# Optimization experiments

Measured on AMD Instinct MI355X. Metric: run time of the kernel, lower is better.

The kernel has to match this reference:

```python
import jax, jax.numpy as jnp
import numpy as np

B, IN, OUT, RANK = 256, 1024, 1024, 16


def setup_inputs() -> dict:
    key = jax.random.key(0)
    k1, k2, k3, k4 = jax.random.split(key, 4)
    std = (0.02 * RANK ** (-0.5)) ** 0.5
    return {
        "input": jax.random.normal(k1, (B, IN), dtype=jnp.float32),
        "coef": jax.random.normal(k2, (B, RANK), dtype=jnp.float32),
        "weight": jax.random.normal(k3, (OUT, IN, RANK), dtype=jnp.float32) * std,
        "bias": jax.random.normal(k4, (OUT, RANK), dtype=jnp.float32) * 0.02,
    }


def reference(input, coef, weight, bias):
    # Per-sample path of MixtureLinear (coef has shape (B, rank), B > 1):
    # out[b,o] = sum_i input[b,i] * sum_r weight[o,i,r] * coef[b,r]
    #          + sum_r bias[o,r] * coef[b,r]
    # Fused form: contract input with weight first -> (B, out, rank), a tiny
    # intermediate, instead of materializing the (B, out, in) combined weight.
    proj = jnp.einsum('bi,oir->bor', input, weight)   # (B, OUT, RANK)
    out = jnp.einsum('bor,br->bo', proj, coef)         # (B, OUT)
    out = out + jnp.einsum('or,br->bo', bias, coef)
    return out
```

## Files before the change

### kernel.cpp

```cpp
#include <hip/hip_runtime.h>
#include <hip/hip_bf16.h>

#define M 256
#define NOUT 1024
#define KTOT 16384
#define RANK 16
#define NKC 32
#define KCHUNK 512
#define BK 32
#define NPH 16
#define BO 64

typedef __attribute__((ext_vector_type(8)))  short bf16x8_t;
typedef __attribute__((ext_vector_type(4)))  float f32x4_t;
typedef __attribute__((ext_vector_type(16))) float f32x16_t;
typedef __attribute__((ext_vector_type(8)))  unsigned short u16x8_t;

static __device__ __forceinline__ unsigned short f2bf(float f) {
  unsigned u = __builtin_bit_cast(unsigned, f);
  u += 0x7FFFu + ((u >> 16) & 1u);
  return (unsigned short)(u >> 16);
}
static __device__ __forceinline__ float bf2f(unsigned short h) {
  unsigned u = ((unsigned)h) << 16;
  return __builtin_bit_cast(float, u);
}
static __device__ __forceinline__ bf16x8_t cvt8(f32x4_t a, f32x4_t b) {
  bf16x8_t r;
  r[0] = (short)f2bf(a[0]); r[1] = (short)f2bf(a[1]);
  r[2] = (short)f2bf(a[2]); r[3] = (short)f2bf(a[3]);
  r[4] = (short)f2bf(b[0]); r[5] = (short)f2bf(b[1]);
  r[6] = (short)f2bf(b[2]); r[7] = (short)f2bf(b[3]);
  return r;
}

__global__ __launch_bounds__(256) void build_x_kernel(
    const float* __restrict__ input, const float* __restrict__ coef,
    unsigned short* __restrict__ X)
{
  int idx = blockIdx.x * 256 + threadIdx.x;
  int b = idx >> 10, i = idx & 1023;
  float in = input[idx];
  const float* c = coef + b * RANK;
  u16x8_t lo, hi;
  #pragma unroll
  for (int r = 0; r < 8; ++r) lo[r] = f2bf(in * c[r]);
  #pragma unroll
  for (int r = 0; r < 8; ++r) hi[r] = f2bf(in * c[8 + r]);
  int chunk = i >> 1;
  int s0 = (i & 1) * 2;
  int sw = b & 3;
  size_t base = ((size_t)chunk * 256 + b) * 32;
  *(u16x8_t*)(X + base + (size_t)((s0    ) ^ sw) * 8) = lo;
  *(u16x8_t*)(X + base + (size_t)((s0 | 1) ^ sw) * 8) = hi;
}

__global__ __launch_bounds__(512, 2) void gemm_kernel(
    const unsigned short* __restrict__ X, const float* __restrict__ W,
    unsigned short* __restrict__ part)
{
  __shared__ unsigned short Xs0[256 * 4 * 8];
  __shared__ unsigned short Xs1[256 * 4 * 8];
  __shared__ float          Wf0[64 * 8 * 4];
  __shared__ float          Wf1[64 * 8 * 4];

  const int tid = threadIdx.x;
  const int w = tid >> 6, lane = tid & 63;
  const int l31 = lane & 31, l5 = lane >> 5;
  const int ow = w & 1, btp = w >> 1;

  const int lin = blockIdx.x;
  const int idx = lin >> 3;
  const int kc = (lin & 7) * 4 + (idx & 3);
  const int ot = idx >> 2;

  const int o0 = ot * BO;
  const int kb0 = kc * KCHUNK;

  f32x16_t acc0 = (f32x16_t)(0.0f), acc1 = (f32x16_t)(0.0f);

  const int wo_ = tid >> 3, ws_ = tid & 7;
  const float* wsrc = W + (size_t)(o0 + wo_) * KTOT + kb0 + ((ws_ ^ (wo_ & 7)) * 4);
  const unsigned short* xbase = X + (size_t)(kc * NPH) * (256 * 32);

  #define SB __builtin_amdgcn_sched_barrier(0);

  #define STAGE(P, XB, WB)                                                   \
    {                                                                        \
      __builtin_amdgcn_global_load_lds(                                      \
          (const __attribute__((address_space(1))) unsigned int*)            \
              (wsrc + (P) * 32),                                             \
          (__attribute__((address_space(3))) unsigned int*)(&WB[tid * 4]),   \
          16, 0, 0);                                                         \
      _Pragma("unroll")                                                      \
      for (int j = 0; j < 2; ++j) {                                          \
        int q = j * 512 + tid;                                               \
        __builtin_amdgcn_global_load_lds(                                    \
            (const __attribute__((address_space(1))) unsigned int*)          \
                (xbase + (size_t)(P) * 8192 + q * 8),                        \
            (__attribute__((address_space(3))) unsigned int*)(&XB[q * 8]),   \
            16, 0, 0);                                                       \
      }                                                                      \
    }

  #define COMPUTE(XB, WB)                                                   \
    {                                                                       \
      _Pragma("unroll")                                                     \
      for (int ks = 0; ks < 2; ++ks) {                                      \
        int o = ow * 32 + l31;                                              \
        f32x4_t a0 = *(const f32x4_t*)                                      \
            &WB[(o * 8 + ((ks * 4 + l5 * 2)     ^ (l31 & 7))) * 4];         \
        f32x4_t a1 = *(const f32x4_t*)                                      \
            &WB[(o * 8 + ((ks * 4 + l5 * 2 + 1) ^ (l31 & 7))) * 4];         \
        bf16x8_t af = cvt8(a0, a1);                                         \
        int b0r = (btp * 2) * 32 + l31;                                     \
        int b1r = (btp * 2 + 1) * 32 + l31;                                 \
        bf16x8_t xf0 = *(const bf16x8_t*)                                   \
            &XB[(b0r * 4 + ((ks * 2 + l5) ^ (l31 & 3))) * 8];               \
        bf16x8_t xf1 = *(const bf16x8_t*)                                   \
            &XB[(b1r * 4 + ((ks * 2 + l5) ^ (l31 & 3))) * 8];               \
        acc0 = __builtin_amdgcn_mfma_f32_32x32x16_bf16(af, xf0, acc0, 0, 0, 0); \
        acc1 = __builtin_amdgcn_mfma_f32_32x32x16_bf16(af, xf1, acc1, 0, 0, 0); \
      }                                                                     \
    }

  #define BAR __syncthreads();

  STAGE(0, Xs0, Wf0) BAR

  STAGE(1,  Xs1, Wf1) SB COMPUTE(Xs0, Wf0) BAR
  STAGE(2,  Xs0, Wf0) SB COMPUTE(Xs1, Wf1) BAR
  STAGE(3,  Xs1, Wf1) SB COMPUTE(Xs0, Wf0) BAR
  STAGE(4,  Xs0, Wf0) SB COMPUTE(Xs1, Wf1) BAR
  STAGE(5,  Xs1, Wf1) SB COMPUTE(Xs0, Wf0) BAR
  STAGE(6,  Xs0, Wf0) SB COMPUTE(Xs1, Wf1) BAR
  STAGE(7,  Xs1, Wf1) SB COMPUTE(Xs0, Wf0) BAR
  STAGE(8,  Xs0, Wf0) SB COMPUTE(Xs1, Wf1) BAR
  STAGE(9,  Xs1, Wf1) SB COMPUTE(Xs0, Wf0) BAR
  STAGE(10, Xs0, Wf0) SB COMPUTE(Xs1, Wf1) BAR
  STAGE(11, Xs1, Wf1) SB COMPUTE(Xs0, Wf0) BAR
  STAGE(12, Xs0, Wf0) SB COMPUTE(Xs1, Wf1) BAR
  STAGE(13, Xs1, Wf1) SB COMPUTE(Xs0, Wf0) BAR
  STAGE(14, Xs0, Wf0) SB COMPUTE(Xs1, Wf1) BAR
  STAGE(15, Xs1, Wf1) SB COMPUTE(Xs0, Wf0) BAR
  COMPUTE(Xs1, Wf1)

  unsigned short* p = part + (size_t)kc * (NOUT * 256);
  #pragma unroll
  for (int q = 0; q < 16; ++q) {
    int o = o0 + ow * 32 + (q & 3) + 8 * (q >> 2) + 4 * l5;
    p[(size_t)o * 256 + (btp * 2) * 32 + l31]     = f2bf(acc0[q]);
    p[(size_t)o * 256 + (btp * 2 + 1) * 32 + l31] = f2bf(acc1[q]);
  }
  #undef STAGE
  #undef COMPUTE
  #undef BAR
  #undef SB
}

__global__ __launch_bounds__(256) void reduce_bias_kernel(
    const unsigned short* __restrict__ part, const float* __restrict__ bias,
    const float* __restrict__ coef, float* __restrict__ out)
{
  __shared__ float lds[8 * 256];
  const int t = threadIdx.x;
  const int o = blockIdx.x * 8 + (t >> 5);
  const int b8 = (t & 31) * 8;

  float s[8];
  #pragma unroll
  for (int j = 0; j < 8; ++j) s[j] = 0.f;

  #pragma unroll 8
  for (int kc = 0; kc < NKC; ++kc) {
    u16x8_t v = *(const u16x8_t*)(part + ((size_t)kc * NOUT + o) * 256 + b8);
    #pragma unroll
    for (int j = 0; j < 8; ++j) s[j] += bf2f(v[j]);
  }

  const f32x4_t* br = (const f32x4_t*)(bias + (size_t)o * RANK);
  f32x4_t b0 = br[0], b1 = br[1], b2 = br[2], b3 = br[3];
  #pragma unroll
  for (int j = 0; j < 8; ++j) {
    const f32x4_t* cr = (const f32x4_t*)(coef + (size_t)(b8 + j) * RANK);
    f32x4_t c0 = cr[0], c1 = cr[1], c2 = cr[2], c3 = cr[3];
    float bb = 0.f;
    #pragma unroll
    for (int e = 0; e < 4; ++e)
      bb += b0[e] * c0[e] + b1[e] * c1[e] + b2[e] * c2[e] + b3[e] * c3[e];
    s[j] += bb;
  }

  f32x4_t v0, v1;
  v0[0] = s[0]; v0[1] = s[1]; v0[2] = s[2]; v0[3] = s[3];
  v1[0] = s[4]; v1[1] = s[5]; v1[2] = s[6]; v1[3] = s[7];
  *(f32x4_t*)&lds[(t >> 5) * 256 + b8]     = v0;
  *(f32x4_t*)&lds[(t >> 5) * 256 + b8 + 4] = v1;
  __syncthreads();

  const int b = t;
  float g[8];
  #pragma unroll
  for (int j = 0; j < 8; ++j) g[j] = lds[j * 256 + b];
  float4* dst = (float4*)(out + (size_t)b * NOUT + blockIdx.x * 8);
  dst[0] = make_float4(g[0], g[1], g[2], g[3]);
  dst[1] = make_float4(g[4], g[5], g[6], g[7]);
}

extern "C" void kernel_launch(void* const* d_in, const int* in_sizes, int n_in,
                              void* d_out, int out_size, void* d_ws, size_t ws_size,
                              hipStream_t stream) {
  const float* input = (const float*)d_in[0];
  const float* coef  = (const float*)d_in[1];
  const float* W     = (const float*)d_in[2];
  const float* bias  = (const float*)d_in[3];
  float* out = (float*)d_out;

  unsigned short* X    = (unsigned short*)d_ws;
  unsigned short* part = (unsigned short*)((char*)d_ws + (size_t)M * KTOT * 2);

  build_x_kernel<<<(M * 1024) / 256, 256, 0, stream>>>(input, coef, X);
  gemm_kernel<<<512, 512, 0, stream>>>(X, W, part);
  reduce_bias_kernel<<<NOUT / 8, 256, 0, stream>>>(part, bias, coef, out);
}
```

Measured before the change: 37.19 us.

## Deepen GEMM pipeline to four LDS stages and halve split-K chunk count

Replaces the double-buffered LDS pipeline with a four-stage ring that keeps three loads in flight, using explicit vmcnt waits and raw s_barrier instead of __syncthreads, and raises wave priority during the MFMA compute. It also doubles the K-chunk per block, so the grid drops from 512 to 256 blocks and the partial buffer read by the reduction shrinks. The aim is to hide global-load latency and cut reduction traffic, at the cost of more LDS per block, which may lower occupancy, and fewer blocks to spread across CUs.

```diff
diff --git a/kernel.cpp b/kernel.cpp
--- a/kernel.cpp
+++ b/kernel.cpp
@@ -5,10 +5,10 @@
 #define NOUT 1024
 #define KTOT 16384
 #define RANK 16
-#define NKC 32
-#define KCHUNK 512
+#define NKC 16
+#define KCHUNK 1024
 #define BK 32
-#define NPH 16
+#define NPH 32
 #define BO 64
 
 typedef __attribute__((ext_vector_type(8)))  short bf16x8_t;
@@ -59,10 +59,8 @@
     const unsigned short* __restrict__ X, const float* __restrict__ W,
     unsigned short* __restrict__ part)
 {
-  __shared__ unsigned short Xs0[256 * 4 * 8];
-  __shared__ unsigned short Xs1[256 * 4 * 8];
-  __shared__ float          Wf0[64 * 8 * 4];
-  __shared__ float          Wf1[64 * 8 * 4];
+  __shared__ unsigned short Xs[4][256 * 4 * 8];
+  __shared__ float          Wf[4][64 * 8 * 4];
 
   const int tid = threadIdx.x;
   const int w = tid >> 6, lane = tid & 63;
@@ -71,8 +69,8 @@
 
   const int lin = blockIdx.x;
   const int idx = lin >> 3;
-  const int kc = (lin & 7) * 4 + (idx & 3);
-  const int ot = idx >> 2;
+  const int kc = (lin & 7) * 2 + (idx & 1);
+  const int ot = idx >> 1;
 
   const int o0 = ot * BO;
   const int kb0 = kc * KCHUNK;
@@ -84,13 +82,15 @@
   const unsigned short* xbase = X + (size_t)(kc * NPH) * (256 * 32);
 
   #define SB __builtin_amdgcn_sched_barrier(0);
-
-  #define STAGE(P, XB, WB)                                                   \
+  #define VM(N) asm volatile("s_waitcnt vmcnt(" #N ")" ::: "memory");
+
+  #define STAGE(P, S)                                                        \
     {                                                                        \
       __builtin_amdgcn_global_load_lds(                                      \
           (const __attribute__((address_space(1))) unsigned int*)            \
-              (wsrc + (P) * 32),                                             \
-          (__attribute__((address_space(3))) unsigned int*)(&WB[tid * 4]),   \
+              (wsrc + (size_t)(P) * 32),                                     \
+          (__attribute__((address_space(3))) unsigned int*)                  \
+              (&Wf[S][tid * 4]),                                             \
           16, 0, 0);                                                         \
       _Pragma("unroll")                                                      \
       for (int j = 0; j < 2; ++j) {                                          \
@@ -98,52 +98,55 @@
         __builtin_amdgcn_global_load_lds(                                    \
             (const __attribute__((address_space(1))) unsigned int*)          \
                 (xbase + (size_t)(P) * 8192 + q * 8),                        \
-            (__attribute__((address_space(3))) unsigned int*)(&XB[q * 8]),   \
+            (__attribute__((address_space(3))) unsigned int*)                \
+                (&Xs[S][q * 8]),                                             \
             16, 0, 0);                                                       \
       }                                                                      \
     }
 
-  #define COMPUTE(XB, WB)                                                   \
-    {                                                                       \
-      _Pragma("unroll")                                                     \
-      for (int ks = 0; ks < 2; ++ks) {                                      \
-        int o = ow * 32 + l31;                                              \
-        f32x4_t a0 = *(const f32x4_t*)                                      \
-            &WB[(o * 8 + ((ks * 4 + l5 * 2)     ^ (l31 & 7))) * 4];         \
-        f32x4_t a1 = *(const f32x4_t*)                                      \
-            &WB[(o * 8 + ((ks * 4 + l5 * 2 + 1) ^ (l31 & 7))) * 4];         \
-        bf16x8_t af = cvt8(a0, a1);                                         \
-        int b0r = (btp * 2) * 32 + l31;                                     \
-        int b1r = (btp * 2 + 1) * 32 + l31;                                 \
-        bf16x8_t xf0 = *(const bf16x8_t*)                                   \
-            &XB[(b0r * 4 + ((ks * 2 + l5) ^ (l31 & 3))) * 8];               \
-        bf16x8_t xf1 = *(const bf16x8_t*)                                   \
-            &XB[(b1r * 4 + ((ks * 2 + l5) ^ (l31 & 3))) * 8];               \
+  #define COMPUTE(S)                                                         \
+    {                                                                        \
+      _Pragma("unroll")                                                      \
+      for (int ks = 0; ks < 2; ++ks) {                                       \
+        int o = ow * 32 + l31;                                               \
+        f32x4_t a0 = *(const f32x4_t*)                                       \
+            &Wf[S][(o * 8 + ((ks * 4 + l5 * 2)     ^ (l31 & 7))) * 4];       \
+        f32x4_t a1 = *(const f32x4_t*)                                       \
+            &Wf[S][(o * 8 + ((ks * 4 + l5 * 2 + 1) ^ (l31 & 7))) * 4];       \
+        bf16x8_t af = cvt8(a0, a1);                                          \
+        int b0r = (btp * 2) * 32 + l31;                                      \
+        int b1r = (btp * 2 + 1) * 32 + l31;                                  \
+        bf16x8_t xf0 = *(const bf16x8_t*)                                    \
+            &Xs[S][(b0r * 4 + ((ks * 2 + l5) ^ (l31 & 3))) * 8];             \
+        bf16x8_t xf1 = *(const bf16x8_t*)                                    \
+            &Xs[S][(b1r * 4 + ((ks * 2 + l5) ^ (l31 & 3))) * 8];             \
         acc0 = __builtin_amdgcn_mfma_f32_32x32x16_bf16(af, xf0, acc0, 0, 0, 0); \
         acc1 = __builtin_amdgcn_mfma_f32_32x32x16_bf16(af, xf1, acc1, 0, 0, 0); \
-      }                                                                     \
+      }                                                                      \
     }
 
-  #define BAR __syncthreads();
-
-  STAGE(0, Xs0, Wf0) BAR
-
-  STAGE(1,  Xs1, Wf1) SB COMPUTE(Xs0, Wf0) BAR
-  STAGE(2,  Xs0, Wf0) SB COMPUTE(Xs1, Wf1) BAR
-  STAGE(3,  Xs1, Wf1) SB COMPUTE(Xs0, Wf0) BAR
-  STAGE(4,  Xs0, Wf0) SB COMPUTE(Xs1, Wf1) BAR
-  STAGE(5,  Xs1, Wf1) SB COMPUTE(Xs0, Wf0) BAR
-  STAGE(6,  Xs0, Wf0) SB COMPUTE(Xs1, Wf1) BAR
-  STAGE(7,  Xs1, Wf1) SB COMPUTE(Xs0, Wf0) BAR
-  STAGE(8,  Xs0, Wf0) SB COMPUTE(Xs1, Wf1) BAR
-  STAGE(9,  Xs1, Wf1) SB COMPUTE(Xs0, Wf0) BAR
-  STAGE(10, Xs0, Wf0) SB COMPUTE(Xs1, Wf1) BAR
-  STAGE(11, Xs1, Wf1) SB COMPUTE(Xs0, Wf0) BAR
-  STAGE(12, Xs0, Wf0) SB COMPUTE(Xs1, Wf1) BAR
-  STAGE(13, Xs1, Wf1) SB COMPUTE(Xs0, Wf0) BAR
-  STAGE(14, Xs0, Wf0) SB COMPUTE(Xs1, Wf1) BAR
-  STAGE(15, Xs1, Wf1) SB COMPUTE(Xs0, Wf0) BAR
-  COMPUTE(Xs1, Wf1)
+  #define ITER(PB, I)                                                        \
+    VM(6) SB                                                                 \
+    __builtin_amdgcn_s_barrier(); SB                                         \
+    STAGE((PB) + (I) + 3, (((I) + 3) & 3)) SB                                \
+    __builtin_amdgcn_s_setprio(1);                                           \
+    COMPUTE(I)                                                               \
+    __builtin_amdgcn_s_setprio(0);
+
+  STAGE(0, 0) STAGE(1, 1) STAGE(2, 2)
+
+  for (int pb = 0; pb < 28; pb += 4) {
+    ITER(pb, 0) ITER(pb, 1) ITER(pb, 2) ITER(pb, 3)
+  }
+
+  VM(6) SB __builtin_amdgcn_s_barrier(); SB STAGE(31, 3) SB
+  __builtin_amdgcn_s_setprio(1); COMPUTE(0) __builtin_amdgcn_s_setprio(0);
+  VM(6) SB __builtin_amdgcn_s_barrier(); SB
+  __builtin_amdgcn_s_setprio(1); COMPUTE(1) __builtin_amdgcn_s_setprio(0);
+  VM(3) SB __builtin_amdgcn_s_barrier(); SB
+  __builtin_amdgcn_s_setprio(1); COMPUTE(2) __builtin_amdgcn_s_setprio(0);
+  VM(0) SB __builtin_amdgcn_s_barrier(); SB
+  COMPUTE(3)
 
   unsigned short* p = part + (size_t)kc * (NOUT * 256);
   #pragma unroll
@@ -154,7 +157,8 @@
   }
   #undef STAGE
   #undef COMPUTE
-  #undef BAR
+  #undef ITER
+  #undef VM
   #undef SB
 }
 
@@ -220,6 +224,6 @@
   unsigned short* part = (unsigned short*)((char*)d_ws + (size_t)M * KTOT * 2);
 
   build_x_kernel<<<(M * 1024) / 256, 256, 0, stream>>>(input, coef, X);
-  gemm_kernel<<<512, 512, 0, stream>>>(X, W, part);
+  gemm_kernel<<<256, 512, 0, stream>>>(X, W, part);
   reduce_bias_kernel<<<NOUT / 8, 256, 0, stream>>>(part, bias, coef, out);
 }
```

Result: slower. 42.50 us (+14.3%).

## Enlarge GEMM output tile and deepen pipeline with register-staged bf16 weights

Applied to the files above, without the earlier changes.

Doubles the output tile to 128 rows per block, so each wave computes a 2x2 set of MFMA tiles and the grid halves to 256 blocks. Weights are now loaded into registers, converted to bf16 once, and written to LDS in MFMA fragment order. X gets a 4-slot ring buffer, the main loop uses explicit waitcnt, a single barrier per phase and setprio, and X's layout is changed to drop the XOR swizzle. The aim is more MFMA reuse per LDS read and to stop reconverting fp32 weights inside the compute loop, at the cost of fewer blocks and more register and LDS pressure.

```diff
diff --git a/kernel.cpp b/kernel.cpp
--- a/kernel.cpp
+++ b/kernel.cpp
@@ -9,7 +9,7 @@
 #define KCHUNK 512
 #define BK 32
 #define NPH 16
-#define BO 64
+#define BO 128
 
 typedef __attribute__((ext_vector_type(8)))  short bf16x8_t;
 typedef __attribute__((ext_vector_type(4)))  float f32x4_t;
@@ -25,13 +25,12 @@
   unsigned u = ((unsigned)h) << 16;
   return __builtin_bit_cast(float, u);
 }
-static __device__ __forceinline__ bf16x8_t cvt8(f32x4_t a, f32x4_t b) {
-  bf16x8_t r;
-  r[0] = (short)f2bf(a[0]); r[1] = (short)f2bf(a[1]);
-  r[2] = (short)f2bf(a[2]); r[3] = (short)f2bf(a[3]);
-  r[4] = (short)f2bf(b[0]); r[5] = (short)f2bf(b[1]);
-  r[6] = (short)f2bf(b[2]); r[7] = (short)f2bf(b[3]);
-  return r;
+static __device__ __forceinline__ void dsw_fn(unsigned short* dst,
+                                              float4 a, float4 b) {
+  u16x8_t hv;
+  hv[0] = f2bf(a.x); hv[1] = f2bf(a.y); hv[2] = f2bf(a.z); hv[3] = f2bf(a.w);
+  hv[4] = f2bf(b.x); hv[5] = f2bf(b.y); hv[6] = f2bf(b.z); hv[7] = f2bf(b.w);
+  *(u16x8_t*)dst = hv;
 }
 
 __global__ __launch_bounds__(256) void build_x_kernel(
@@ -47,114 +46,127 @@
   for (int r = 0; r < 8; ++r) lo[r] = f2bf(in * c[r]);
   #pragma unroll
   for (int r = 0; r < 8; ++r) hi[r] = f2bf(in * c[8 + r]);
-  int chunk = i >> 1;
-  int s0 = (i & 1) * 2;
-  int sw = b & 3;
-  size_t base = ((size_t)chunk * 256 + b) * 32;
-  *(u16x8_t*)(X + base + (size_t)((s0    ) ^ sw) * 8) = lo;
-  *(u16x8_t*)(X + base + (size_t)((s0 | 1) ^ sw) * 8) = hi;
+  size_t base = (size_t)(i >> 1) * 8192 + (size_t)((i & 1) * 2) * 2048 + b * 8;
+  *(u16x8_t*)(X + base)        = lo;
+  *(u16x8_t*)(X + base + 2048) = hi;
 }
 
 __global__ __launch_bounds__(512, 2) void gemm_kernel(
     const unsigned short* __restrict__ X, const float* __restrict__ W,
     unsigned short* __restrict__ part)
 {
-  __shared__ unsigned short Xs0[256 * 4 * 8];
-  __shared__ unsigned short Xs1[256 * 4 * 8];
-  __shared__ float          Wf0[64 * 8 * 4];
-  __shared__ float          Wf1[64 * 8 * 4];
+  __shared__ __align__(16) unsigned short Xs[4][8192];
+  __shared__ __align__(16) unsigned short Wl[2][4096];
 
   const int tid = threadIdx.x;
-  const int w = tid >> 6, lane = tid & 63;
+  const int wid = tid >> 6, lane = tid & 63;
   const int l31 = lane & 31, l5 = lane >> 5;
-  const int ow = w & 1, btp = w >> 1;
+  const int wr = wid >> 2, wc = wid & 3;
 
   const int lin = blockIdx.x;
-  const int idx = lin >> 3;
-  const int kc = (lin & 7) * 4 + (idx & 3);
-  const int ot = idx >> 2;
+  const int kc = (lin & 7) * 4 + ((lin >> 3) & 3);
+  const int ot = lin >> 5;
 
   const int o0 = ot * BO;
   const int kb0 = kc * KCHUNK;
 
-  f32x16_t acc0 = (f32x16_t)(0.0f), acc1 = (f32x16_t)(0.0f);
-
-  const int wo_ = tid >> 3, ws_ = tid & 7;
-  const float* wsrc = W + (size_t)(o0 + wo_) * KTOT + kb0 + ((ws_ ^ (wo_ & 7)) * 4);
-  const unsigned short* xbase = X + (size_t)(kc * NPH) * (256 * 32);
+  f32x16_t a00 = (f32x16_t)(0.0f), a01 = (f32x16_t)(0.0f);
+  f32x16_t a10 = (f32x16_t)(0.0f), a11 = (f32x16_t)(0.0f);
+
+  const int wrow = tid >> 2, wq = tid & 3;
+  const float* wgp = W + (size_t)(o0 + wrow) * KTOT + kb0 + wq * 8;
+  const int widx = (((tid >> 7) * 4 + wq) * 32 + (wrow & 31)) * 8;
+  const unsigned short* xbase = X + (size_t)kc * NPH * 8192;
+
+  float4 wA0, wA1, wB0, wB1, wC0, wC1;
 
   #define SB __builtin_amdgcn_sched_barrier(0);
 
-  #define STAGE(P, XB, WB)                                                   \
-    {                                                                        \
-      __builtin_amdgcn_global_load_lds(                                      \
-          (const __attribute__((address_space(1))) unsigned int*)            \
-              (wsrc + (P) * 32),                                             \
-          (__attribute__((address_space(3))) unsigned int*)(&WB[tid * 4]),   \
-          16, 0, 0);                                                         \
-      _Pragma("unroll")                                                      \
+  #define LOADW(S, P)                                                        \
+    { w##S##0 = *(const float4*)(wgp + (P) * 32);                            \
+      w##S##1 = *(const float4*)(wgp + (P) * 32 + 4); }
+
+  #define DSW(S, PB) dsw_fn(&Wl[PB][widx], w##S##0, w##S##1);
+
+  #define STX(P, SL)                                                         \
+    { _Pragma("unroll")                                                      \
       for (int j = 0; j < 2; ++j) {                                          \
         int q = j * 512 + tid;                                               \
         __builtin_amdgcn_global_load_lds(                                    \
             (const __attribute__((address_space(1))) unsigned int*)          \
                 (xbase + (size_t)(P) * 8192 + q * 8),                        \
-            (__attribute__((address_space(3))) unsigned int*)(&XB[q * 8]),   \
+            (__attribute__((address_space(3))) unsigned int*)                \
+                (&Xs[SL][q * 8]),                                            \
             16, 0, 0);                                                       \
-      }                                                                      \
-    }
-
-  #define COMPUTE(XB, WB)                                                   \
-    {                                                                       \
-      _Pragma("unroll")                                                     \
+      } }
+
+  #define COMP(XS, PB)                                                      \
+    { _Pragma("unroll")                                                     \
       for (int ks = 0; ks < 2; ++ks) {                                      \
-        int o = ow * 32 + l31;                                              \
-        f32x4_t a0 = *(const f32x4_t*)                                      \
-            &WB[(o * 8 + ((ks * 4 + l5 * 2)     ^ (l31 & 7))) * 4];         \
-        f32x4_t a1 = *(const f32x4_t*)                                      \
-            &WB[(o * 8 + ((ks * 4 + l5 * 2 + 1) ^ (l31 & 7))) * 4];         \
-        bf16x8_t af = cvt8(a0, a1);                                         \
-        int b0r = (btp * 2) * 32 + l31;                                     \
-        int b1r = (btp * 2 + 1) * 32 + l31;                                 \
+        bf16x8_t af0 = *(const bf16x8_t*)                                   \
+            &Wl[PB][(((wr * 2 + 0) * 4 + ks * 2 + l5) * 32 + l31) * 8];     \
+        bf16x8_t af1 = *(const bf16x8_t*)                                   \
+            &Wl[PB][(((wr * 2 + 1) * 4 + ks * 2 + l5) * 32 + l31) * 8];     \
         bf16x8_t xf0 = *(const bf16x8_t*)                                   \
-            &XB[(b0r * 4 + ((ks * 2 + l5) ^ (l31 & 3))) * 8];               \
+            &Xs[XS][((ks * 2 + l5) * 256 + wc * 64 + l31) * 8];             \
         bf16x8_t xf1 = *(const bf16x8_t*)                                   \
-            &XB[(b1r * 4 + ((ks * 2 + l5) ^ (l31 & 3))) * 8];               \
-        acc0 = __builtin_amdgcn_mfma_f32_32x32x16_bf16(af, xf0, acc0, 0, 0, 0); \
-        acc1 = __builtin_amdgcn_mfma_f32_32x32x16_bf16(af, xf1, acc1, 0, 0, 0); \
-      }                                                                     \
-    }
-
-  #define BAR __syncthreads();
-
-  STAGE(0, Xs0, Wf0) BAR
-
-  STAGE(1,  Xs1, Wf1) SB COMPUTE(Xs0, Wf0) BAR
-  STAGE(2,  Xs0, Wf0) SB COMPUTE(Xs1, Wf1) BAR
-  STAGE(3,  Xs1, Wf1) SB COMPUTE(Xs0, Wf0) BAR
-  STAGE(4,  Xs0, Wf0) SB COMPUTE(Xs1, Wf1) BAR
-  STAGE(5,  Xs1, Wf1) SB COMPUTE(Xs0, Wf0) BAR
-  STAGE(6,  Xs0, Wf0) SB COMPUTE(Xs1, Wf1) BAR
-  STAGE(7,  Xs1, Wf1) SB COMPUTE(Xs0, Wf0) BAR
-  STAGE(8,  Xs0, Wf0) SB COMPUTE(Xs1, Wf1) BAR
-  STAGE(9,  Xs1, Wf1) SB COMPUTE(Xs0, Wf0) BAR
-  STAGE(10, Xs0, Wf0) SB COMPUTE(Xs1, Wf1) BAR
-  STAGE(11, Xs1, Wf1) SB COMPUTE(Xs0, Wf0) BAR
-  STAGE(12, Xs0, Wf0) SB COMPUTE(Xs1, Wf1) BAR
-  STAGE(13, Xs1, Wf1) SB COMPUTE(Xs0, Wf0) BAR
-  STAGE(14, Xs0, Wf0) SB COMPUTE(Xs1, Wf1) BAR
-  STAGE(15, Xs1, Wf1) SB COMPUTE(Xs0, Wf0) BAR
-  COMPUTE(Xs1, Wf1)
-
-  unsigned short* p = part + (size_t)kc * (NOUT * 256);
+            &Xs[XS][((ks * 2 + l5) * 256 + wc * 64 + 32 + l31) * 8];        \
+        a00 = __builtin_amdgcn_mfma_f32_32x32x16_bf16(af0, xf0, a00, 0, 0, 0); \
+        a01 = __builtin_amdgcn_mfma_f32_32x32x16_bf16(af0, xf1, a01, 0, 0, 0); \
+        a10 = __builtin_amdgcn_mfma_f32_32x32x16_bf16(af1, xf0, a10, 0, 0, 0); \
+        a11 = __builtin_amdgcn_mfma_f32_32x32x16_bf16(af1, xf1, a11, 0, 0, 0); \
+      } }
+
+  #define PHASE(P, CS, NS, XC, XI, DOW, DOX)                                 \
+    asm volatile("s_waitcnt vmcnt(6)" ::: "memory"); SB                      \
+    DSW(CS, (P) & 1)                                                         \
+    asm volatile("s_waitcnt lgkmcnt(0)" ::: "memory"); SB                    \
+    __builtin_amdgcn_s_barrier(); SB                                         \
+    if (DOW) { LOADW(NS, (P) + 2) }                                          \
+    if (DOX) { STX((P) + 3, XI) }                                            \
+    SB                                                                       \
+    __builtin_amdgcn_s_setprio(1);                                           \
+    COMP(XC, (P) & 1)                                                        \
+    __builtin_amdgcn_s_setprio(0);
+
+  STX(0, 0) SB
+  LOADW(A, 0) SB
+  STX(1, 1) SB
+  LOADW(B, 1) SB
+  STX(2, 2) SB
+
+  PHASE(0,  A, C, 0, 3, 1, 1)
+  PHASE(1,  B, A, 1, 0, 1, 1)
+  PHASE(2,  C, B, 2, 1, 1, 1)
+  PHASE(3,  A, C, 3, 2, 1, 1)
+  PHASE(4,  B, A, 0, 3, 1, 1)
+  PHASE(5,  C, B, 1, 0, 1, 1)
+  PHASE(6,  A, C, 2, 1, 1, 1)
+  PHASE(7,  B, A, 3, 2, 1, 1)
+  PHASE(8,  C, B, 0, 3, 1, 1)
+  PHASE(9,  A, C, 1, 0, 1, 1)
+  PHASE(10, B, A, 2, 1, 1, 1)
+  PHASE(11, C, B, 3, 2, 1, 1)
+  PHASE(12, A, C, 0, 3, 1, 1)
+  PHASE(13, B, A, 1, 0, 1, 0)
+  PHASE(14, C, B, 2, 1, 0, 0)
+  PHASE(15, A, C, 3, 2, 0, 0)
+
+  unsigned short* pp = part + (size_t)kc * (NOUT * 256);
   #pragma unroll
   for (int q = 0; q < 16; ++q) {
-    int o = o0 + ow * 32 + (q & 3) + 8 * (q >> 2) + 4 * l5;
-    p[(size_t)o * 256 + (btp * 2) * 32 + l31]     = f2bf(acc0[q]);
-    p[(size_t)o * 256 + (btp * 2 + 1) * 32 + l31] = f2bf(acc1[q]);
+    int oo = o0 + wr * 64 + (q & 3) + 8 * (q >> 2) + 4 * l5;
+    int cb = wc * 64 + l31;
+    pp[(size_t)oo * 256 + cb]             = f2bf(a00[q]);
+    pp[(size_t)oo * 256 + cb + 32]        = f2bf(a01[q]);
+    pp[(size_t)(oo + 32) * 256 + cb]      = f2bf(a10[q]);
+    pp[(size_t)(oo + 32) * 256 + cb + 32] = f2bf(a11[q]);
   }
-  #undef STAGE
-  #undef COMPUTE
-  #undef BAR
+  #undef LOADW
+  #undef DSW
+  #undef STX
+  #undef COMP
+  #undef PHASE
   #undef SB
 }
 
@@ -220,6 +232,6 @@
   unsigned short* part = (unsigned short*)((char*)d_ws + (size_t)M * KTOT * 2);
 
   build_x_kernel<<<(M * 1024) / 256, 256, 0, stream>>>(input, coef, X);
-  gemm_kernel<<<512, 512, 0, stream>>>(X, W, part);
+  gemm_kernel<<<256, 512, 0, stream>>>(X, W, part);
   reduce_bias_kernel<<<NOUT / 8, 256, 0, stream>>>(part, bias, coef, out);
 }
```

After: 39.57 us. 6.4% more time.
